# Performance work log

Hardware: AMD Instinct MI355X
Metric: run time of the kernel (lower is better)

## Reference

```python
import jax, jax.numpy as jnp
import numpy as np

N_NODES = 50000
N_EDGES = 600000
HIDDEN = 128
NUM_CLASSES = 5
NUM_NODE_FEATURES = 3
NUM_GRAPHS = 128


def setup_inputs() -> dict:
    key = jax.random.key(0)
    ks = jax.random.split(key, 12)
    x = jax.random.normal(ks[0], (N_NODES, NUM_NODE_FEATURES), dtype=jnp.float32)
    edge_index = jax.random.randint(ks[1], (2, N_EDGES), 0, N_NODES, dtype=jnp.int64)
    batch = jnp.sort(jax.random.randint(ks[2], (N_NODES,), 0, NUM_GRAPHS, dtype=jnp.int64))
    def glorot(k, fan_in, fan_out):
        s = jnp.sqrt(6.0 / (fan_in + fan_out)).astype(jnp.float32)
        return jax.random.uniform(k, (fan_in, fan_out), jnp.float32, -s, s)
    return {
        "x": x,
        "edge_index": edge_index,
        "batch": batch,
        "W1": glorot(ks[3], NUM_NODE_FEATURES, HIDDEN), "b1": jnp.zeros((HIDDEN,), jnp.float32),
        "W2": glorot(ks[4], HIDDEN, HIDDEN), "b2": jnp.zeros((HIDDEN,), jnp.float32),
        "W3": glorot(ks[5], HIDDEN, HIDDEN), "b3": jnp.zeros((HIDDEN,), jnp.float32),
        "Wl": glorot(ks[6], HIDDEN, NUM_CLASSES), "bl": jnp.zeros((NUM_CLASSES,), jnp.float32),
    }


def _gcn_norm(edge_index, n_nodes):
    # Add self loops, compute symmetric normalization D^-1/2 (A+I) D^-1/2.
    loops = jnp.arange(n_nodes, dtype=edge_index.dtype)
    src = jnp.concatenate([edge_index[0], loops])
    dst = jnp.concatenate([edge_index[1], loops])
    ones = jnp.ones(src.shape[0], dtype=jnp.float32)
    deg = jax.ops.segment_sum(ones, dst, num_segments=n_nodes)
    dis = jnp.where(deg > 0, jax.lax.rsqrt(jnp.maximum(deg, 1.0)), 0.0)
    norm = dis[src] * dis[dst]  # [E + N]
    return src, dst, norm


def _gcn_conv(h, W, b, src, dst, norm, n_nodes):
    h = h @ W                              # [N, out]
    msg = h[src] * norm[:, None]           # gather + scale: [E+N, out]
    out = jax.ops.segment_sum(msg, dst, num_segments=n_nodes)  # scatter-add
    return out + b


def reference(x, edge_index, batch, W1, b1, W2, b2, W3, b3, Wl, bl):
    n = x.shape[0]
    src, dst, norm = _gcn_norm(edge_index, n)
    h = jax.nn.relu(_gcn_conv(x, W1, b1, src, dst, norm, n))
    h = jax.nn.relu(_gcn_conv(h, W2, b2, src, dst, norm, n))
    h = jax.nn.relu(_gcn_conv(h, W3, b3, src, dst, norm, n))
    # global_mean_pool over graphs
    sums = jax.ops.segment_sum(h, batch, num_segments=NUM_GRAPHS)
    cnts = jax.ops.segment_sum(jnp.ones((n,), jnp.float32), batch, num_segments=NUM_GRAPHS)
    fingerprint = sums / jnp.maximum(cnts, 1.0)[:, None]  # [G, HIDDEN]
    # dropout is identity in eval mode
    return fingerprint @ Wl + bl  # [G, NUM_CLASSES]
```

## Files before the change

### kernel.cpp

```cpp
#include <hip/hip_runtime.h>

#define N_NODES   50000
#define N_EDGES   600000
#define HID       128
#define N_GRAPHS  128
#define N_CLASSES 5
#define PREP_BLK  ((N_NODES + 255) / 256)
#define RSTRIDE   40

__global__ void k_fill2(const int* __restrict__ src, const int* __restrict__ dst,
                        int* __restrict__ cursor, unsigned short* __restrict__ col, int E) {
    int i = blockIdx.x * blockDim.x + threadIdx.x;
    if (i < E) {
        int d = dst[i];
        int pos = atomicAdd(&cursor[d], 1);
        if (pos < RSTRIDE) col[d * RSTRIDE + pos] = (unsigned short)src[i];
    }
}

__global__ void k_prep(const int* __restrict__ cursor, const float* __restrict__ x,
                       float* __restrict__ dis, float4* __restrict__ xs,
                       const int* __restrict__ batch, int* __restrict__ gcnt, int n) {
    if (blockIdx.x == gridDim.x - 1) {
        __shared__ int s[N_GRAPHS + 1];
        int t = threadIdx.x;
        if (t <= N_GRAPHS) {
            int lo = 0, hi = n;
            while (lo < hi) {
                int mid = (lo + hi) >> 1;
                if (batch[mid] < t) lo = mid + 1; else hi = mid;
            }
            s[t] = lo;
        }
        __syncthreads();
        if (t < N_GRAPHS) gcnt[t] = s[t + 1] - s[t];
        return;
    }
    int i = blockIdx.x * 256 + threadIdx.x;
    if (i < n) {
        float dd = 1.0f / sqrtf((float)cursor[i] + 1.0f);
        dis[i] = dd;
        float4 o;
        o.x = dd * x[i * 3 + 0];
        o.y = dd * x[i * 3 + 1];
        o.z = dd * x[i * 3 + 2];
        o.w = 0.f;
        xs[i] = o;
    }
}

__global__ __launch_bounds__(256) void k_agg3l1(const float4* __restrict__ xs,
                                                const float* __restrict__ dis,
                                                const int* __restrict__ deg,
                                                const unsigned short* __restrict__ col,
                                                const float* __restrict__ W1,
                                                const float* __restrict__ b1,
                                                float* __restrict__ out) {
    __shared__ float Wls[3 * HID];
    __shared__ float bls[HID];
    int t = threadIdx.x;
    for (int i = t; i < 3 * HID; i += 256) Wls[i] = W1[i];
    for (int i = t; i < HID; i += 256) bls[i] = b1[i];
    __syncthreads();

    int g = t >> 2;
    int f = t & 3;
    int d = blockIdx.x * 64 + g;
    if (d >= N_NODES) return;
    const float* xsf = (const float*)xs;
    int j0 = d * RSTRIDE;
    int j1 = j0 + min(deg[d], RSTRIDE);
    float a0 = xsf[(size_t)d * 4 + f];
    float a1 = 0.f, a2 = 0.f, a3 = 0.f;
    int j = j0;
    for (; j + 3 < j1; j += 4) {
        int s0 = col[j], s1 = col[j + 1], s2 = col[j + 2], s3 = col[j + 3];
        a0 += xsf[(size_t)s0 * 4 + f];
        a1 += xsf[(size_t)s1 * 4 + f];
        a2 += xsf[(size_t)s2 * 4 + f];
        a3 += xsf[(size_t)s3 * 4 + f];
    }
    for (; j < j1; ++j)
        a0 += xsf[(size_t)col[j] * 4 + f];
    float val = dis[d] * ((a0 + a1) + (a2 + a3));

    int base = (t & 63) & ~3;
    float av0 = __shfl(val, base + 0);
    float av1 = __shfl(val, base + 1);
    float av2 = __shfl(val, base + 2);

    const float* w0 = &Wls[0 * HID];
    const float* w1 = &Wls[1 * HID];
    const float* w2 = &Wls[2 * HID];
    int c0 = f * 32;
#pragma unroll
    for (int c4 = 0; c4 < 8; ++c4) {
        int c = c0 + c4 * 4;
        float4 o;
        o.x = fmaxf(fmaf(av2, w2[c + 0], fmaf(av1, w1[c + 0], fmaf(av0, w0[c + 0], bls[c + 0]))), 0.f);
        o.y = fmaxf(fmaf(av2, w2[c + 1], fmaf(av1, w1[c + 1], fmaf(av0, w0[c + 1], bls[c + 1]))), 0.f);
        o.z = fmaxf(fmaf(av2, w2[c + 2], fmaf(av1, w1[c + 2], fmaf(av0, w0[c + 2], bls[c + 2]))), 0.f);
        o.w = fmaxf(fmaf(av2, w2[c + 3], fmaf(av1, w1[c + 3], fmaf(av0, w0[c + 3], bls[c + 3]))), 0.f);
        *(float4*)&out[(size_t)d * HID + c] = o;
    }
}

__global__ __launch_bounds__(512, 2) void k_gemm128(const float* __restrict__ h,
                                                    const float* __restrict__ W,
                                                    const float* __restrict__ dis,
                                                    float* __restrict__ out, int n) {
    __shared__ float Ws[HID * HID];
    int t  = threadIdx.x;
    int tc = t & 31;
    int tr = t >> 5;
    int row0 = blockIdx.x * 128 + tr * 8;
    if (row0 + 8 > n) row0 = n - 8;

    {
        const float4* wg = (const float4*)W;
        float4* wsv = (float4*)Ws;
#pragma unroll
        for (int i = 0; i < 8; ++i)
            wsv[i * 512 + t] = wg[i * 512 + t];
    }

    const float* hp = h + (size_t)row0 * HID;

    float4 ha[8], hb[8];
#pragma unroll
    for (int r = 0; r < 8; ++r) ha[r] = *(const float4*)(hp + r * HID);

    float acc[8][4];
#pragma unroll
    for (int r = 0; r < 8; ++r)
#pragma unroll
        for (int c = 0; c < 4; ++c) acc[r][c] = 0.f;

    __syncthreads();

    for (int k0 = 0; k0 < HID; k0 += 8) {
#pragma unroll
        for (int r = 0; r < 8; ++r) hb[r] = *(const float4*)(hp + r * HID + k0 + 4);
#pragma unroll
        for (int kk = 0; kk < 4; ++kk) {
            float4 wv = *(const float4*)&Ws[(k0 + kk) * HID + tc * 4];
#pragma unroll
            for (int r = 0; r < 8; ++r) {
                float hv = kk == 0 ? ha[r].x : kk == 1 ? ha[r].y : kk == 2 ? ha[r].z : ha[r].w;
                acc[r][0] = fmaf(hv, wv.x, acc[r][0]);
                acc[r][1] = fmaf(hv, wv.y, acc[r][1]);
                acc[r][2] = fmaf(hv, wv.z, acc[r][2]);
                acc[r][3] = fmaf(hv, wv.w, acc[r][3]);
            }
        }
        if (k0 + 8 < HID) {
#pragma unroll
            for (int r = 0; r < 8; ++r) ha[r] = *(const float4*)(hp + r * HID + k0 + 8);
        }
#pragma unroll
        for (int kk = 0; kk < 4; ++kk) {
            float4 wv = *(const float4*)&Ws[(k0 + 4 + kk) * HID + tc * 4];
#pragma unroll
            for (int r = 0; r < 8; ++r) {
                float hv = kk == 0 ? hb[r].x : kk == 1 ? hb[r].y : kk == 2 ? hb[r].z : hb[r].w;
                acc[r][0] = fmaf(hv, wv.x, acc[r][0]);
                acc[r][1] = fmaf(hv, wv.y, acc[r][1]);
                acc[r][2] = fmaf(hv, wv.z, acc[r][2]);
                acc[r][3] = fmaf(hv, wv.w, acc[r][3]);
            }
        }
    }

#pragma unroll
    for (int r = 0; r < 8; ++r) {
        int row = row0 + r;
        if (row < n) {
            float dd = dis[row];
            float4 o;
            o.x = dd * acc[r][0]; o.y = dd * acc[r][1];
            o.z = dd * acc[r][2]; o.w = dd * acc[r][3];
            *(float4*)&out[(size_t)row * HID + tc * 4] = o;
        }
    }
}

__global__ __launch_bounds__(256) void k_agg(const float* __restrict__ t,
                                             const float* __restrict__ dis,
                                             const int* __restrict__ deg,
                                             const unsigned short* __restrict__ col,
                                             const float* __restrict__ bias,
                                             float* __restrict__ out) {
    int lane = threadIdx.x & 31;
    int wid  = threadIdx.x >> 5;
    int d = blockIdx.x * 8 + wid;
    if (d >= N_NODES) return;
    const float4* t4 = (const float4*)t;
    float4 bv = ((const float4*)bias)[lane];
    float dd = dis[d];
    int j0 = d * RSTRIDE;
    int j1 = j0 + min(deg[d], RSTRIDE);
    float4 self = t4[(size_t)d * 32 + lane];
    float x0 = self.x, y0 = self.y, z0 = self.z, w0 = self.w;
    float x1 = 0.f, y1 = 0.f, z1 = 0.f, w1 = 0.f;
    float x2 = 0.f, y2 = 0.f, z2 = 0.f, w2 = 0.f;
    float x3 = 0.f, y3 = 0.f, z3 = 0.f, w3 = 0.f;
    int j = j0;
    for (; j + 3 < j1; j += 4) {
        ushort4 sv = *(const ushort4*)&col[j];
        float4 v0 = t4[(size_t)sv.x * 32 + lane];
        float4 v1 = t4[(size_t)sv.y * 32 + lane];
        float4 v2 = t4[(size_t)sv.z * 32 + lane];
        float4 v3 = t4[(size_t)sv.w * 32 + lane];
        x0 += v0.x; y0 += v0.y; z0 += v0.z; w0 += v0.w;
        x1 += v1.x; y1 += v1.y; z1 += v1.z; w1 += v1.w;
        x2 += v2.x; y2 += v2.y; z2 += v2.z; w2 += v2.w;
        x3 += v3.x; y3 += v3.y; z3 += v3.z; w3 += v3.w;
    }
    for (; j < j1; ++j) {
        int s = col[j];
        float4 v = t4[(size_t)s * 32 + lane];
        x0 += v.x; y0 += v.y; z0 += v.z; w0 += v.w;
    }
    float sx = (x0 + x1) + (x2 + x3);
    float sy = (y0 + y1) + (y2 + y3);
    float sz = (z0 + z1) + (z2 + z3);
    float sw = (w0 + w1) + (w2 + w3);
    float4 o;
    o.x = fmaxf(fmaf(dd, sx, bv.x), 0.f);
    o.y = fmaxf(fmaf(dd, sy, bv.y), 0.f);
    o.z = fmaxf(fmaf(dd, sz, bv.z), 0.f);
    o.w = fmaxf(fmaf(dd, sw, bv.w), 0.f);
    ((float4*)out)[(size_t)d * 32 + lane] = o;
}

__global__ __launch_bounds__(256) void k_aggpool(const float* __restrict__ t,
                                                 const float* __restrict__ dis,
                                                 const int* __restrict__ deg,
                                                 const unsigned short* __restrict__ col,
                                                 const float* __restrict__ bias,
                                                 const int* __restrict__ batch,
                                                 float* __restrict__ fpsum) {
    __shared__ float sh[8][HID];
    __shared__ int bg[8];
    int lane = threadIdx.x & 31;
    int wid  = threadIdx.x >> 5;
    int d = blockIdx.x * 8 + wid;
    bool valid = (d < N_NODES);
    if (lane == 0) bg[wid] = valid ? batch[d] : -1;
    __syncthreads();
    int g0 = bg[0];

    float4 o = make_float4(0.f, 0.f, 0.f, 0.f);
    if (valid) {
        const float4* t4 = (const float4*)t;
        float4 bv = ((const float4*)bias)[lane];
        float dd = dis[d];
        int j0 = d * RSTRIDE;
        int j1 = j0 + min(deg[d], RSTRIDE);
        float4 self = t4[(size_t)d * 32 + lane];
        float x0 = self.x, y0 = self.y, z0 = self.z, w0 = self.w;
        float x1 = 0.f, y1 = 0.f, z1 = 0.f, w1 = 0.f;
        float x2 = 0.f, y2 = 0.f, z2 = 0.f, w2 = 0.f;
        float x3 = 0.f, y3 = 0.f, z3 = 0.f, w3 = 0.f;
        int j = j0;
        for (; j + 3 < j1; j += 4) {
            ushort4 sv = *(const ushort4*)&col[j];
            float4 v0 = t4[(size_t)sv.x * 32 + lane];
            float4 v1 = t4[(size_t)sv.y * 32 + lane];
            float4 v2 = t4[(size_t)sv.z * 32 + lane];
            float4 v3 = t4[(size_t)sv.w * 32 + lane];
            x0 += v0.x; y0 += v0.y; z0 += v0.z; w0 += v0.w;
            x1 += v1.x; y1 += v1.y; z1 += v1.z; w1 += v1.w;
            x2 += v2.x; y2 += v2.y; z2 += v2.z; w2 += v2.w;
            x3 += v3.x; y3 += v3.y; z3 += v3.z; w3 += v3.w;
        }
        for (; j < j1; ++j) {
            int s = col[j];
            float4 v = t4[(size_t)s * 32 + lane];
            x0 += v.x; y0 += v.y; z0 += v.z; w0 += v.w;
        }
        float sx = (x0 + x1) + (x2 + x3);
        float sy = (y0 + y1) + (y2 + y3);
        float sz = (z0 + z1) + (z2 + z3);
        float sw = (w0 + w1) + (w2 + w3);
        o.x = fmaxf(fmaf(dd, sx, bv.x), 0.f);
        o.y = fmaxf(fmaf(dd, sy, bv.y), 0.f);
        o.z = fmaxf(fmaf(dd, sz, bv.z), 0.f);
        o.w = fmaxf(fmaf(dd, sw, bv.w), 0.f);
    }

    if (valid) {
        if (bg[wid] == g0) {
            *(float4*)&sh[wid][lane * 4] = o;
        } else {
            int g = bg[wid];
            atomicAdd(&fpsum[g * HID + lane * 4 + 0], o.x);
            atomicAdd(&fpsum[g * HID + lane * 4 + 1], o.y);
            atomicAdd(&fpsum[g * HID + lane * 4 + 2], o.z);
            atomicAdd(&fpsum[g * HID + lane * 4 + 3], o.w);
        }
    }
    __syncthreads();
    int f = threadIdx.x;
    if (f < HID) {
        float s = 0.f;
#pragma unroll
        for (int w = 0; w < 8; ++w)
            if (bg[w] == g0) s += sh[w][f];
        atomicAdd(&fpsum[g0 * HID + f], s);
    }
}

__global__ void k_final(const float* __restrict__ fpsum, const int* __restrict__ gcnt,
                        const float* __restrict__ Wl, const float* __restrict__ bl,
                        float* __restrict__ out) {
    int idx = blockIdx.x * blockDim.x + threadIdx.x;
    if (idx >= N_GRAPHS * N_CLASSES) return;
    int g = idx / N_CLASSES, c = idx % N_CLASSES;
    float inv = 1.0f / (float)max(gcnt[g], 1);
    float acc = bl[c];
    for (int f = 0; f < HID; ++f)
        acc = fmaf(fpsum[g * HID + f] * inv, Wl[f * N_CLASSES + c], acc);
    out[idx] = acc;
}

extern "C" void kernel_launch(void* const* d_in, const int* in_sizes, int n_in,
                              void* d_out, int out_size, void* d_ws, size_t ws_size,
                              hipStream_t stream) {
    const float* x     = (const float*)d_in[0];
    const int*   ei    = (const int*)d_in[1];
    const int*   batch = (const int*)d_in[2];
    const float* W1 = (const float*)d_in[3];
    const float* b1 = (const float*)d_in[4];
    const float* W2 = (const float*)d_in[5];
    const float* b2 = (const float*)d_in[6];
    const float* W3 = (const float*)d_in[7];
    const float* b3 = (const float*)d_in[8];
    const float* Wl = (const float*)d_in[9];
    const float* bl = (const float*)d_in[10];
    float* out = (float*)d_out;

    const int N = N_NODES, E = N_EDGES;
    const int* srcp = ei;
    const int* dstp = ei + E;

    char* ws = (char*)d_ws;
    size_t off = 0;
    auto alloc = [&](size_t bytes) -> void* {
        void* p = ws + off;
        off += (bytes + 255) & ~(size_t)255;
        return p;
    };
    int*   cursor = (int*)alloc((size_t)N * 4);
    float* fpsum  = (float*)alloc((size_t)N_GRAPHS * HID * 4);
    size_t zero_bytes = off;
    int*   gcnt  = (int*)alloc((size_t)N_GRAPHS * 4);
    float* dis   = (float*)alloc((size_t)N * 4);
    unsigned short* col = (unsigned short*)alloc((size_t)N * RSTRIDE * 2);
    float* bufA  = (float*)alloc((size_t)N * HID * 4);
    float* bufB  = (float*)alloc((size_t)N * HID * 4);
    float4* xs   = (float4*)alloc((size_t)N * 16);

    hipMemsetAsync(d_ws, 0, zero_bytes, stream);

    const int tpb = 256;
    k_fill2<<<(E + tpb - 1) / tpb, tpb, 0, stream>>>(srcp, dstp, cursor, col, E);
    k_prep<<<PREP_BLK + 1, 256, 0, stream>>>(cursor, x, dis, xs, batch, gcnt, N);

    k_agg3l1<<<(N + 63) / 64, 256, 0, stream>>>(xs, dis, cursor, col, W1, b1, bufB);
    k_gemm128<<<(N + 127) / 128, 512, 0, stream>>>(bufB, W2, dis, bufA, N);
    k_agg<<<(N + 7) / 8, 256, 0, stream>>>(bufA, dis, cursor, col, b2, bufB);
    k_gemm128<<<(N + 127) / 128, 512, 0, stream>>>(bufB, W3, dis, bufA, N);
    k_aggpool<<<(N + 7) / 8, 256, 0, stream>>>(bufA, dis, cursor, col, b3, batch, fpsum);
    k_final<<<(N_GRAPHS * N_CLASSES + tpb - 1) / tpb, tpb, 0, stream>>>(fpsum, gcnt, Wl, bl, out);
}
```

Baseline: 304.9 us.

## Replace shared-memory GEMM with smaller-tile register GEMM reading W from cache

The dense 128x128 GEMM no longer stages W into 64KB of LDS. Each thread now reads W directly from global memory through the cache and computes a 4x4 tile instead of 8x4. Blocks shrink to 256 threads over 32 rows, which raises the block count and occupancy and removes the LDS fill and barrier. The cost is more global/L2 traffic for W, less register reuse per loaded value, and an unguarded tail store. That store is safe only because row0 is clamped and N is a multiple of 4.

Result: slower. 344.5 us (+13.0%).

```diff
diff --git a/kernel.cpp b/kernel.cpp
--- a/kernel.cpp
+++ b/kernel.cpp
@@ -105,82 +105,64 @@
     }
 }
 
-__global__ __launch_bounds__(512, 2) void k_gemm128(const float* __restrict__ h,
+__global__ __launch_bounds__(256, 8) void k_gemm32r(const float* __restrict__ h,
                                                     const float* __restrict__ W,
                                                     const float* __restrict__ dis,
                                                     float* __restrict__ out, int n) {
-    __shared__ float Ws[HID * HID];
     int t  = threadIdx.x;
     int tc = t & 31;
     int tr = t >> 5;
-    int row0 = blockIdx.x * 128 + tr * 8;
-    if (row0 + 8 > n) row0 = n - 8;
-
-    {
-        const float4* wg = (const float4*)W;
-        float4* wsv = (float4*)Ws;
-#pragma unroll
-        for (int i = 0; i < 8; ++i)
-            wsv[i * 512 + t] = wg[i * 512 + t];
-    }
+    int row0 = blockIdx.x * 32 + tr * 4;
+    if (row0 + 4 > n) row0 = n - 4;
 
     const float* hp = h + (size_t)row0 * HID;
-
-    float4 ha[8], hb[8];
-#pragma unroll
-    for (int r = 0; r < 8; ++r) ha[r] = *(const float4*)(hp + r * HID);
-
-    float acc[8][4];
-#pragma unroll
-    for (int r = 0; r < 8; ++r)
+    const float* wp = W + tc * 4;
+
+    float acc[4][4];
+#pragma unroll
+    for (int r = 0; r < 4; ++r)
 #pragma unroll
         for (int c = 0; c < 4; ++c) acc[r][c] = 0.f;
 
-    __syncthreads();
-
-    for (int k0 = 0; k0 < HID; k0 += 8) {
-#pragma unroll
-        for (int r = 0; r < 8; ++r) hb[r] = *(const float4*)(hp + r * HID + k0 + 4);
+    for (int k0 = 0; k0 < HID; k0 += 4) {
+        float4 ha0 = *(const float4*)(hp + 0 * HID + k0);
+        float4 ha1 = *(const float4*)(hp + 1 * HID + k0);
+        float4 ha2 = *(const float4*)(hp + 2 * HID + k0);
+        float4 ha3 = *(const float4*)(hp + 3 * HID + k0);
 #pragma unroll
         for (int kk = 0; kk < 4; ++kk) {
-            float4 wv = *(const float4*)&Ws[(k0 + kk) * HID + tc * 4];
-#pragma unroll
-            for (int r = 0; r < 8; ++r) {
-                float hv = kk == 0 ? ha[r].x : kk == 1 ? ha[r].y : kk == 2 ? ha[r].z : ha[r].w;
-                acc[r][0] = fmaf(hv, wv.x, acc[r][0]);
-                acc[r][1] = fmaf(hv, wv.y, acc[r][1]);
-                acc[r][2] = fmaf(hv, wv.z, acc[r][2]);
-                acc[r][3] = fmaf(hv, wv.w, acc[r][3]);
-            }
-        }
-        if (k0 + 8 < HID) {
-#pragma unroll
-            for (int r = 0; r < 8; ++r) ha[r] = *(const float4*)(hp + r * HID + k0 + 8);
-        }
-#pragma unroll
-        for (int kk = 0; kk < 4; ++kk) {
-            float4 wv = *(const float4*)&Ws[(k0 + 4 + kk) * HID + tc * 4];
-#pragma unroll
-            for (int r = 0; r < 8; ++r) {
-                float hv = kk == 0 ? hb[r].x : kk == 1 ? hb[r].y : kk == 2 ? hb[r].z : hb[r].w;
-                acc[r][0] = fmaf(hv, wv.x, acc[r][0]);
-                acc[r][1] = fmaf(hv, wv.y, acc[r][1]);
-                acc[r][2] = fmaf(hv, wv.z, acc[r][2]);
-                acc[r][3] = fmaf(hv, wv.w, acc[r][3]);
-            }
-        }
-    }
-
-#pragma unroll
-    for (int r = 0; r < 8; ++r) {
+            float4 wv = *(const float4*)(wp + (k0 + kk) * HID);
+            float h0 = kk == 0 ? ha0.x : kk == 1 ? ha0.y : kk == 2 ? ha0.z : ha0.w;
+            float h1 = kk == 0 ? ha1.x : kk == 1 ? ha1.y : kk == 2 ? ha1.z : ha1.w;
+            float h2 = kk == 0 ? ha2.x : kk == 1 ? ha2.y : kk == 2 ? ha2.z : ha2.w;
+            float h3 = kk == 0 ? ha3.x : kk == 1 ? ha3.y : kk == 2 ? ha3.z : ha3.w;
+            acc[0][0] = fmaf(h0, wv.x, acc[0][0]);
+            acc[0][1] = fmaf(h0, wv.y, acc[0][1]);
+            acc[0][2] = fmaf(h0, wv.z, acc[0][2]);
+            acc[0][3] = fmaf(h0, wv.w, acc[0][3]);
+            acc[1][0] = fmaf(h1, wv.x, acc[1][0]);
+            acc[1][1] = fmaf(h1, wv.y, acc[1][1]);
+            acc[1][2] = fmaf(h1, wv.z, acc[1][2]);
+            acc[1][3] = fmaf(h1, wv.w, acc[1][3]);
+            acc[2][0] = fmaf(h2, wv.x, acc[2][0]);
+            acc[2][1] = fmaf(h2, wv.y, acc[2][1]);
+            acc[2][2] = fmaf(h2, wv.z, acc[2][2]);
+            acc[2][3] = fmaf(h2, wv.w, acc[2][3]);
+            acc[3][0] = fmaf(h3, wv.x, acc[3][0]);
+            acc[3][1] = fmaf(h3, wv.y, acc[3][1]);
+            acc[3][2] = fmaf(h3, wv.z, acc[3][2]);
+            acc[3][3] = fmaf(h3, wv.w, acc[3][3]);
+        }
+    }
+
+#pragma unroll
+    for (int r = 0; r < 4; ++r) {
         int row = row0 + r;
-        if (row < n) {
-            float dd = dis[row];
-            float4 o;
-            o.x = dd * acc[r][0]; o.y = dd * acc[r][1];
-            o.z = dd * acc[r][2]; o.w = dd * acc[r][3];
-            *(float4*)&out[(size_t)row * HID + tc * 4] = o;
-        }
+        float dd = dis[row];
+        float4 o;
+        o.x = dd * acc[r][0]; o.y = dd * acc[r][1];
+        o.z = dd * acc[r][2]; o.w = dd * acc[r][3];
+        *(float4*)&out[(size_t)row * HID + tc * 4] = o;
     }
 }
 
@@ -367,10 +349,11 @@
     k_fill2<<<(E + tpb - 1) / tpb, tpb, 0, stream>>>(srcp, dstp, cursor, col, E);
     k_prep<<<PREP_BLK + 1, 256, 0, stream>>>(cursor, x, dis, xs, batch, gcnt, N);
 
+    const int gemm_grid = (N + 31) / 32;
     k_agg3l1<<<(N + 63) / 64, 256, 0, stream>>>(xs, dis, cursor, col, W1, b1, bufB);
-    k_gemm128<<<(N + 127) / 128, 512, 0, stream>>>(bufB, W2, dis, bufA, N);
+    k_gemm32r<<<gemm_grid, 256, 0, stream>>>(bufB, W2, dis, bufA, N);
     k_agg<<<(N + 7) / 8, 256, 0, stream>>>(bufA, dis, cursor, col, b2, bufB);
-    k_gemm128<<<(N + 127) / 128, 512, 0, stream>>>(bufB, W3, dis, bufA, N);
+    k_gemm32r<<<gemm_grid, 256, 0, stream>>>(bufB, W3, dis, bufA, N);
     k_aggpool<<<(N + 7) / 8, 256, 0, stream>>>(bufA, dis, cursor, col, b3, batch, fpsum);
     k_final<<<(N_GRAPHS * N_CLASSES + tpb - 1) / tpb, tpb, 0, stream>>>(fpsum, gcnt, Wl, bl, out);
 }
```
